# Kernel tuning notes

Measured on AMD Instinct MI355X. Metric: run time of the kernel, lower is better.

Reference implementation:

```python
import jax, jax.numpy as jnp
import numpy as np

B, S, D, H = 2, 2048, 2048, 16
DH = D // H  # 128


def setup_inputs() -> dict:
    key = jax.random.key(0)
    ks = jax.random.split(key, 7)
    x = jax.random.normal(ks[0], (B, S, D), dtype=jnp.float32)
    # causal mask [b, s, s], True = attend
    mask = jnp.broadcast_to(jnp.tril(jnp.ones((S, S), dtype=bool)), (B, S, S))
    scale = 1.0 / np.sqrt(D)
    Wq = jax.random.normal(ks[1], (D, H, DH), dtype=jnp.float32) * scale
    Wk = jax.random.normal(ks[2], (D, 1, DH), dtype=jnp.float32) * scale
    Wv = jax.random.normal(ks[3], (D, 1, DH), dtype=jnp.float32) * scale
    Wo = jax.random.normal(ks[4], (H, DH, D), dtype=jnp.float32) * scale
    bo = jnp.zeros((D,), dtype=jnp.float32)
    return {"x": x, "mask": mask, "Wq": Wq, "Wk": Wk, "Wv": Wv, "Wo": Wo, "bo": bo}


def reference(x, mask, Wq, Wk, Wv, Wo, bo):
    # projections: q [b,s,h,dh]; k,v [b,s,1,dh] (single shared KV head)
    q = jnp.einsum("bsd,dhe->bshe", x, Wq)
    k = jnp.einsum("bsd,dhe->bshe", x, Wk)[:, :, 0, :]  # [b,s,dh]
    v = jnp.einsum("bsd,dhe->bshe", x, Wv)[:, :, 0, :]  # [b,s,dh]
    # scores [b,h,s,s] with 1/sqrt(d_head) scaling
    scores = jnp.einsum("bqhe,bke->bhqk", q, k) / jnp.sqrt(
        jnp.asarray(q.shape[-1], dtype=q.dtype)
    )
    big_neg = jnp.finfo(scores.dtype).min
    scores = jnp.where(mask[:, None, :, :], scores, big_neg)
    probs = jax.nn.softmax(scores, axis=-1)
    attn = jnp.einsum("bhqk,bke->bhqe", probs, v)  # [b,h,s,dh]
    # output projection contracting (head, d_head) -> d_state, with bias
    out = jnp.einsum("bhqe,hed->bqd", attn, Wo) + bo
    return out
```

## Files before the change

kernel.cpp:

```cpp
#include <hip/hip_runtime.h>
#include <cmath>
#include <cstdint>

typedef __bf16 bf16;
typedef __bf16 bf16x8 __attribute__((ext_vector_type(8)));
typedef __bf16 bf16x4 __attribute__((ext_vector_type(4)));
typedef float f32x4 __attribute__((ext_vector_type(4)));

#define SDIM 2048
#define DDIM 2048
#define NQKV 2304
#define DH   128

__device__ __forceinline__ void glds16(const bf16* g, bf16* l) {
    __builtin_amdgcn_global_load_lds(
        (const __attribute__((address_space(1))) void*)g,
        (__attribute__((address_space(3))) void*)l, 16, 0, 0);
}

#define MEMFENCE() asm volatile("" ::: "memory")
#define SBAR() do { MEMFENCE(); __builtin_amdgcn_s_barrier(); MEMFENCE(); } while (0)

__global__ __launch_bounds__(256) void prep_kernel(const float* __restrict__ x,
                                                   const float* __restrict__ Wq,
                                                   const float* __restrict__ Wk,
                                                   const float* __restrict__ Wv,
                                                   const float* __restrict__ Wo,
                                                   bf16* __restrict__ xb,
                                                   bf16* __restrict__ Wqkv_t,
                                                   bf16* __restrict__ Wo_t) {
    __shared__ float tile[32][33];
    int bx = blockIdx.x;
    if (bx < 8192) {
        int i = bx * 256 + threadIdx.x;
        float4 v = reinterpret_cast<const float4*>(x)[i];
        bf16x4 o;
        o[0] = (bf16)v.x; o[1] = (bf16)v.y; o[2] = (bf16)v.z; o[3] = (bf16)v.w;
        reinterpret_cast<bf16x4*>(xb)[i] = o;
        return;
    }
    bx -= 8192;
    const float* src; bf16* dst; int srcN; int t;
    if (bx < 4096)      { src = Wq; dst = Wqkv_t;                      srcN = 2048; t = bx; }
    else if (bx < 4352) { src = Wk; dst = Wqkv_t + (size_t)2048*2048;  srcN = 128;  t = bx - 4096; }
    else if (bx < 4608) { src = Wv; dst = Wqkv_t + (size_t)2176*2048;  srcN = 128;  t = bx - 4352; }
    else                { src = Wo; dst = Wo_t;                        srcN = 2048; t = bx - 4608; }
    const int srcK = 2048;
    int ntx = srcN >> 5;
    int n0 = (t % ntx) * 32, k0 = (t / ntx) * 32;
    int tx = threadIdx.x & 31;
    int ty = threadIdx.x >> 5;
    for (int i = 0; i < 4; i++)
        tile[ty + i*8][tx] = src[(size_t)(k0 + ty + i*8) * srcN + n0 + tx];
    __syncthreads();
    for (int i = 0; i < 4; i++)
        dst[(size_t)(n0 + ty + i*8) * srcK + k0 + tx] = (bf16)tile[tx][ty + i*8];
}

template<int WRITE_F32, int BNW, int WRITE_VT>
__global__ __launch_bounds__(512, 2) void gemm8_kernel(const bf16* __restrict__ A,
                                                       const bf16* __restrict__ Bt,
                                                       void* __restrict__ Cout,
                                                       const float* __restrict__ bias,
                                                       bf16* __restrict__ Vt,
                                                       int N) {
    constexpr int K  = 2048;
    constexpr int NT = 32;
    constexpr int BN = 64 * BNW;
    constexpr int BHALF = BN * 32;
    __shared__ bf16 smem[32768 + 4 * BHALF];

    const int tid  = threadIdx.x;
    const int wave = tid >> 6, lane = tid & 63;
    const int quad = lane >> 4, l15 = lane & 15;
    const int wm = wave >> 2, wn = wave & 3;
    const int tm = blockIdx.x * 256, tn = blockIdx.y * BN;

    const int r0  = wave * 32 + (lane >> 2);
    const int r0b = (BNW == 4) ? r0 : (wave * 16 + (lane >> 2));
    const int cs  = (lane & 3) ^ ((lane >> 3) & 3);
    const bf16* Ag = A  + (size_t)(tm + r0)  * K + cs * 8;
    const bf16* Bg = Bt + (size_t)(tn + r0b) * K + cs * 8;
    bf16* Asl = smem + wave * 1024;
    bf16* Bsl = smem + 32768 + wave * ((BNW == 4) ? 1024 : 512);

    auto STAGE_A = [&](int t, int kh) {
        if (t < NT) {
            const bf16* s = Ag + t * 64 + kh * 32;
            bf16* d = Asl + (t & 1) * 16384 + kh * 8192;
            glds16(s, d);
            glds16(s + 16 * K, d + 512);
        }
    };
    auto STAGE_B = [&](int t, int kh) {
        if (t < NT) {
            const bf16* s = Bg + t * 64 + kh * 32;
            bf16* d = Bsl + (t & 1) * (2 * BHALF) + kh * BHALF;
            glds16(s, d);
            if constexpr (BNW == 4) glds16(s + 16 * K, d + 512);
        }
    };

    const int rsw  = (l15 >> 1) & 3;
    const int aoff = (wm * 128      + l15) * 32 + ((quad ^ rsw) * 8);
    const int boff = (wn * 16 * BNW + l15) * 32 + ((quad ^ rsw) * 8);

    f32x4 acc[8][BNW];
#pragma unroll
    for (int m = 0; m < 8; m++)
#pragma unroll
        for (int n = 0; n < BNW; n++) acc[m][n] = (f32x4)0.0f;

    STAGE_A(0, 0); STAGE_B(0, 0);
    STAGE_A(0, 1); STAGE_B(0, 1);
    STAGE_A(1, 0); STAGE_B(1, 0);
    if constexpr (BNW == 4) asm volatile("s_waitcnt vmcnt(4)" ::: "memory");
    else                    asm volatile("s_waitcnt vmcnt(3)" ::: "memory");
    SBAR();

    bf16x8 av[4], bv[BNW];
    for (int t = 0; t < NT; ++t) {
        const int buf = t & 1;
        const bf16* Sa = smem + buf * 16384;
        const bf16* Sb = smem + 32768 + buf * (2 * BHALF);

#pragma unroll
        for (int m = 0; m < 4; m++) av[m] = *reinterpret_cast<const bf16x8*>(Sa + aoff + m * 512);
#pragma unroll
        for (int n = 0; n < BNW; n++) bv[n] = *reinterpret_cast<const bf16x8*>(Sb + boff + n * 512);
        STAGE_A(t + 1, 1);
        SBAR();
        __builtin_amdgcn_s_setprio(1);
#pragma unroll
        for (int m = 0; m < 4; m++)
#pragma unroll
            for (int n = 0; n < BNW; n++)
                acc[m][n] = __builtin_amdgcn_mfma_f32_16x16x32_bf16(av[m], bv[n], acc[m][n], 0, 0, 0);
        __builtin_amdgcn_s_setprio(0);
        SBAR();

#pragma unroll
        for (int m = 0; m < 4; m++) av[m] = *reinterpret_cast<const bf16x8*>(Sa + aoff + 2048 + m * 512);
        STAGE_B(t + 1, 1);
        SBAR();
        __builtin_amdgcn_s_setprio(1);
#pragma unroll
        for (int m = 0; m < 4; m++)
#pragma unroll
            for (int n = 0; n < BNW; n++)
                acc[4 + m][n] = __builtin_amdgcn_mfma_f32_16x16x32_bf16(av[m], bv[n], acc[4 + m][n], 0, 0, 0);
        __builtin_amdgcn_s_setprio(0);
        if (t + 1 < NT) {
            if constexpr (BNW == 4) asm volatile("s_waitcnt vmcnt(8)" ::: "memory");
            else                    asm volatile("s_waitcnt vmcnt(6)" ::: "memory");
        } else {
            asm volatile("s_waitcnt vmcnt(0)" ::: "memory");
        }
        SBAR();

#pragma unroll
        for (int m = 0; m < 4; m++) av[m] = *reinterpret_cast<const bf16x8*>(Sa + 8192 + aoff + m * 512);
#pragma unroll
        for (int n = 0; n < BNW; n++) bv[n] = *reinterpret_cast<const bf16x8*>(Sb + BHALF + boff + n * 512);
        STAGE_A(t + 2, 0);
        SBAR();
        __builtin_amdgcn_s_setprio(1);
#pragma unroll
        for (int m = 0; m < 4; m++)
#pragma unroll
            for (int n = 0; n < BNW; n++)
                acc[m][n] = __builtin_amdgcn_mfma_f32_16x16x32_bf16(av[m], bv[n], acc[m][n], 0, 0, 0);
        __builtin_amdgcn_s_setprio(0);
        SBAR();

#pragma unroll
        for (int m = 0; m < 4; m++) av[m] = *reinterpret_cast<const bf16x8*>(Sa + 8192 + aoff + 2048 + m * 512);
        STAGE_B(t + 2, 0);
        SBAR();
        __builtin_amdgcn_s_setprio(1);
#pragma unroll
        for (int m = 0; m < 4; m++)
#pragma unroll
            for (int n = 0; n < BNW; n++)
                acc[4 + m][n] = __builtin_amdgcn_mfma_f32_16x16x32_bf16(av[m], bv[n], acc[4 + m][n], 0, 0, 0);
        __builtin_amdgcn_s_setprio(0);
        if (t + 2 < NT) {
            if constexpr (BNW == 4) asm volatile("s_waitcnt vmcnt(4)" ::: "memory");
            else                    asm volatile("s_waitcnt vmcnt(3)" ::: "memory");
        } else {
            asm volatile("s_waitcnt vmcnt(0)" ::: "memory");
        }
        SBAR();
    }

#pragma unroll
    for (int m = 0; m < 8; m++)
#pragma unroll
        for (int n = 0; n < BNW; n++) {
#pragma unroll
            for (int r = 0; r < 4; r++) {
                int row = tm + wm * 128 + m * 16 + quad * 4 + r;
                int col = tn + wn * 16 * BNW + n * 16 + l15;
                float v = acc[m][n][r];
                if (WRITE_F32)
                    reinterpret_cast<float*>(Cout)[(size_t)row * N + col] = v + bias[col];
                else
                    reinterpret_cast<bf16*>(Cout)[(size_t)row * N + col] = (bf16)v;
            }
            if constexpr (WRITE_VT) {
                if (tn == 2048 && wn >= 2) {
                    int col  = tn + wn * 16 * BNW + n * 16 + l15;
                    int d    = col - 2176;
                    int row0 = tm + wm * 128 + m * 16 + quad * 4;
                    int bb   = row0 >> 11;
                    int s0v  = row0 & 2047;
                    int pp0  = (s0v & ~63) | (s0v & 32) | ((s0v & 12) << 1) | ((s0v & 16) >> 2);
                    bf16x4 vv;
                    vv[0] = (bf16)acc[m][n][0]; vv[1] = (bf16)acc[m][n][1];
                    vv[2] = (bf16)acc[m][n][2]; vv[3] = (bf16)acc[m][n][3];
                    *reinterpret_cast<bf16x4*>(Vt + ((size_t)bb * DH + d) * SDIM + pp0) = vv;
                }
            }
        }
}

__global__ __launch_bounds__(512, 4) void flash_kernel(const bf16* __restrict__ QKV,
                                                       const bf16* __restrict__ Vt,
                                                       bf16* __restrict__ attn) {
    __shared__ __align__(16) bf16 KVS[32768];
    const int tid  = threadIdx.x;
    const int wave = tid >> 6, lane = tid & 63;
    const int quad = lane >> 4, l15 = lane & 15;
    const int bx = blockIdx.x;
    const int u  = (bx < 256) ? bx : bx - 256;
    const int qs = (bx < 256) ? (255 - (u >> 1)) : (u >> 1);
    const int b  = u & 1;
    const int q  = qs * 8 + wave;
    const size_t rowbase = (size_t)b * SDIM;
    const bf16* Vtb = Vt + (size_t)b * DH * SDIM;
    const float scale = 0.088388347648318447f;

    const int s0 = wave, s1 = wave + 8;
    const int krow0 = s0*4 + quad, krow1 = s1*4 + quad;
    const bf16* kp0 = QKV + (rowbase + krow0) * NQKV + 2048 + ((l15 ^ (krow0 & 15)) * 8);
    const bf16* kp1 = QKV + (rowbase + krow1) * NQKV + 2048 + ((l15 ^ (krow1 & 15)) * 8);
    const int vrow0 = s0*8 + (lane >> 3), vrow1 = s1*8 + (lane >> 3);
    const bf16* vp0 = Vtb + (size_t)vrow0 * SDIM + (((lane & 7) ^ (vrow0 & 7)) * 8);
    const bf16* vp1 = Vtb + (size_t)vrow1 * SDIM + (((lane & 7) ^ (vrow1 & 7)) * 8);

    bf16x8 qf[4];
    {
        const bf16* qp = QKV + (rowbase + q) * NQKV + l15 * DH + quad * 8;
#pragma unroll
        for (int kk = 0; kk < 4; kk++) qf[kk] = *reinterpret_cast<const bf16x8*>(qp + kk * 32);
    }

    f32x4 acc[8];
#pragma unroll
    for (int d = 0; d < 8; d++) acc[d] = (f32x4)0.0f;
    float l_s = 0.0f;

    const int ntiles = (qs >> 3) + 1;

    glds16(kp0, KVS + s0 * 512);         glds16(kp1, KVS + s1 * 512);
    glds16(vp0, KVS + 16384 + s0 * 512); glds16(vp1, KVS + 16384 + s1 * 512);
    kp0 += 64 * NQKV; kp1 += 64 * NQKV; vp0 += 64; vp1 += 64;

    for (int t = 0; t < ntiles; t++) {
        asm volatile("s_waitcnt vmcnt(2)" ::: "memory");
        SBAR();
        if (t + 1 < ntiles) {
            bf16* kb = KVS + ((t + 1) & 1) * 8192;
            glds16(kp0, kb + s0 * 512); glds16(kp1, kb + s1 * 512);
            kp0 += 64 * NQKV; kp1 += 64 * NQKV;
        }
        const bf16* Ks  = KVS + (t & 1) * 8192;
        const bf16* Vts = KVS + 16384 + (t & 1) * 8192;
        const int key0 = t * 64;

        f32x4 sc[4];
#pragma unroll
        for (int c = 0; c < 4; c++) sc[c] = (f32x4)0.0f;
        __builtin_amdgcn_s_setprio(1);
#pragma unroll
        for (int c = 0; c < 4; c++)
#pragma unroll
            for (int kk = 0; kk < 4; kk++) {
                bf16x8 kf = *reinterpret_cast<const bf16x8*>(
                    Ks + (c*16 + l15) * 128 + (((kk*4 + quad) ^ l15) * 8));
                sc[c] = __builtin_amdgcn_mfma_f32_16x16x32_bf16(kf, qf[kk], sc[c], 0, 0, 0);
            }
        __builtin_amdgcn_s_setprio(0);

        bf16x8 pa[2];
        {
            const bool tail = (key0 + 63 > q);
            float ps = 0.0f;
#pragma unroll
            for (int c = 0; c < 4; c++)
#pragma unroll
                for (int r = 0; r < 4; r++) {
                    int key = key0 + c*16 + quad*4 + r;
                    float pv = (tail && key > q) ? 0.0f : __expf(sc[c][r] * scale);
                    ps += pv;
                    pa[c >> 1][(c & 1)*4 + r] = (bf16)pv;
                }
            l_s += ps;
        }

        if (t + 1 < ntiles) asm volatile("s_waitcnt vmcnt(2)" ::: "memory");
        else                asm volatile("s_waitcnt vmcnt(0)" ::: "memory");

        __builtin_amdgcn_s_setprio(1);
#pragma unroll
        for (int kk2 = 0; kk2 < 2; kk2++)
#pragma unroll
            for (int dd = 0; dd < 8; dd++) {
                bf16x8 vf = *reinterpret_cast<const bf16x8*>(
                    Vts + (dd*16 + l15) * 64 + (((kk2*4 + quad) ^ (l15 & 7)) * 8));
                acc[dd] = __builtin_amdgcn_mfma_f32_16x16x32_bf16(pa[kk2], vf, acc[dd], 0, 0, 0);
            }
        __builtin_amdgcn_s_setprio(0);

        if (t + 1 < ntiles) {
            bf16* vb = KVS + 16384 + ((t + 1) & 1) * 8192;
            glds16(vp0, vb + s0 * 512); glds16(vp1, vb + s1 * 512);
            vp0 += 64; vp1 += 64;
        }
    }

    __syncthreads();

    float linv;
    {
        float v = l_s;
        v += __shfl_xor(v, 16);
        v += __shfl_xor(v, 32);
        linv = 1.0f / v;
    }

    bf16* Ow = KVS + wave * 2048;
#pragma unroll
    for (int r = 0; r < 4; r++) {
        float inv = __shfl(linv, quad*4 + r);
#pragma unroll
        for (int dd = 0; dd < 8; dd++)
            Ow[(quad*4 + r)*128 + dd*16 + l15] = (bf16)(acc[dd][r] * inv);
    }
    const int orow = lane >> 2;
    const int ocol = (lane & 3) * 8;
    bf16* ob = attn + (rowbase + q) * (size_t)DDIM;
#pragma unroll
    for (int it = 0; it < 4; it++)
        *reinterpret_cast<uint4*>(ob + orow * DH + ocol + it*32) =
            *reinterpret_cast<const uint4*>(Ow + orow * 128 + ocol + it*32);
}

extern "C" void kernel_launch(void* const* d_in, const int* in_sizes, int n_in,
                              void* d_out, int out_size, void* d_ws, size_t ws_size,
                              hipStream_t stream) {
    const float* x  = (const float*)d_in[0];
    const float* Wq = (const float*)d_in[2];
    const float* Wk = (const float*)d_in[3];
    const float* Wv = (const float*)d_in[4];
    const float* Wo = (const float*)d_in[5];
    const float* bo = (const float*)d_in[6];
    float* out = (float*)d_out;

    char* ws = (char*)d_ws;
    bf16* xb     = (bf16*)(ws);
    bf16* Wqkv_t = (bf16*)(ws + 16777216);
    bf16* Wo_t   = (bf16*)(ws + 26214400);
    bf16* QKV    = (bf16*)(ws + 34603008);
    bf16* attn   = (bf16*)(ws + 53477376);
    bf16* Vtb    = (bf16*)(ws + 70254592);
    (void)ws_size; (void)in_sizes; (void)n_in; (void)out_size;

    prep_kernel<<<16896, 256, 0, stream>>>(x, Wq, Wk, Wv, Wo, xb, Wqkv_t, Wo_t);
    gemm8_kernel<0, 4, 1><<<dim3(16, 9), 512, 0, stream>>>(xb, Wqkv_t, (void*)QKV, nullptr, Vtb, 2304);
    flash_kernel<<<512, 512, 0, stream>>>(QKV, Vtb, attn);
    gemm8_kernel<1, 2, 0><<<dim3(16, 16), 512, 0, stream>>>(attn, Wo_t, (void*)out, bo, nullptr, 2048);
}
```

Measured before the change: 281.8 us.

## Restructure GEMM main loop into a triple-buffered K=32 pipeline with one barrier

The GEMM main loop changes from a double-buffered 64-wide K step, split into four sub-phases with many barriers, to a triple-buffered 32-wide K step. Each iteration issues the async global-to-LDS load two steps ahead, runs all 8xBNW MFMAs, then waits and crosses a single barrier. This aims to cut barrier and synchronisation overhead and keep more loads in flight. The cost is more loop iterations, a different LDS footprint, and register pressure from holding 8 A fragments at once.

```diff
diff --git a/kernel.cpp b/kernel.cpp
--- a/kernel.cpp
+++ b/kernel.cpp
@@ -58,52 +58,45 @@
 }
 
 template<int WRITE_F32, int BNW, int WRITE_VT>
-__global__ __launch_bounds__(512, 2) void gemm8_kernel(const bf16* __restrict__ A,
+__global__ __launch_bounds__(512, 2) void gemm9_kernel(const bf16* __restrict__ A,
                                                        const bf16* __restrict__ Bt,
                                                        void* __restrict__ Cout,
                                                        const float* __restrict__ bias,
                                                        bf16* __restrict__ Vt,
                                                        int N) {
-    constexpr int K  = 2048;
-    constexpr int NT = 32;
-    constexpr int BN = 64 * BNW;
-    constexpr int BHALF = BN * 32;
-    __shared__ bf16 smem[32768 + 4 * BHALF];
+    constexpr int K    = 2048;
+    constexpr int NT   = 64;
+    constexpr int ABUF = 8192;
+    constexpr int BBUF = BNW * 2048;
+    constexpr int GPT  = 2 + (BNW >> 1);
+    __shared__ bf16 smem[3 * ABUF + 3 * BBUF];
 
     const int tid  = threadIdx.x;
     const int wave = tid >> 6, lane = tid & 63;
     const int quad = lane >> 4, l15 = lane & 15;
     const int wm = wave >> 2, wn = wave & 3;
-    const int tm = blockIdx.x * 256, tn = blockIdx.y * BN;
-
-    const int r0  = wave * 32 + (lane >> 2);
-    const int r0b = (BNW == 4) ? r0 : (wave * 16 + (lane >> 2));
-    const int cs  = (lane & 3) ^ ((lane >> 3) & 3);
-    const bf16* Ag = A  + (size_t)(tm + r0)  * K + cs * 8;
-    const bf16* Bg = Bt + (size_t)(tn + r0b) * K + cs * 8;
-    bf16* Asl = smem + wave * 1024;
-    bf16* Bsl = smem + 32768 + wave * ((BNW == 4) ? 1024 : 512);
-
-    auto STAGE_A = [&](int t, int kh) {
-        if (t < NT) {
-            const bf16* s = Ag + t * 64 + kh * 32;
-            bf16* d = Asl + (t & 1) * 16384 + kh * 8192;
-            glds16(s, d);
-            glds16(s + 16 * K, d + 512);
-        }
+    const int tm = blockIdx.x * 256, tn = blockIdx.y * (64 * BNW);
+
+    const int rr = wave * 16 + (lane >> 2);
+    const int cs = (lane & 3) ^ ((lane >> 3) & 3);
+    const bf16* Ag = A  + (size_t)(tm + rr) * K + cs * 8;
+    const bf16* Bg = Bt + (size_t)(tn + rr) * K + cs * 8;
+    bf16* Asl = smem + wave * 512;
+    bf16* Bsl = smem + 3 * ABUF + wave * 512;
+
+    auto STAGE = [&](int t, int s3) {
+        const bf16* sa = Ag + t * 32;
+        bf16* da = Asl + s3 * ABUF;
+        glds16(sa, da);
+        glds16(sa + 128 * K, da + 4096);
+        const bf16* sb = Bg + t * 32;
+        bf16* db = Bsl + s3 * BBUF;
+        glds16(sb, db);
+        if constexpr (BNW == 4) glds16(sb + 128 * K, db + 4096);
     };
-    auto STAGE_B = [&](int t, int kh) {
-        if (t < NT) {
-            const bf16* s = Bg + t * 64 + kh * 32;
-            bf16* d = Bsl + (t & 1) * (2 * BHALF) + kh * BHALF;
-            glds16(s, d);
-            if constexpr (BNW == 4) glds16(s + 16 * K, d + 512);
-        }
-    };
 
     const int rsw  = (l15 >> 1) & 3;
-    const int aoff = (wm * 128      + l15) * 32 + ((quad ^ rsw) * 8);
-    const int boff = (wn * 16 * BNW + l15) * 32 + ((quad ^ rsw) * 8);
+    const int coff = (quad ^ rsw) * 8;
 
     f32x4 acc[8][BNW];
 #pragma unroll
@@ -111,79 +104,34 @@
 #pragma unroll
         for (int n = 0; n < BNW; n++) acc[m][n] = (f32x4)0.0f;
 
-    STAGE_A(0, 0); STAGE_B(0, 0);
-    STAGE_A(0, 1); STAGE_B(0, 1);
-    STAGE_A(1, 0); STAGE_B(1, 0);
+    STAGE(0, 0);
+    STAGE(1, 1);
     if constexpr (BNW == 4) asm volatile("s_waitcnt vmcnt(4)" ::: "memory");
     else                    asm volatile("s_waitcnt vmcnt(3)" ::: "memory");
     SBAR();
 
-    bf16x8 av[4], bv[BNW];
+    int b3 = 0, s3 = 2;
     for (int t = 0; t < NT; ++t) {
-        const int buf = t & 1;
-        const bf16* Sa = smem + buf * 16384;
-        const bf16* Sb = smem + 32768 + buf * (2 * BHALF);
-
-#pragma unroll
-        for (int m = 0; m < 4; m++) av[m] = *reinterpret_cast<const bf16x8*>(Sa + aoff + m * 512);
-#pragma unroll
-        for (int n = 0; n < BNW; n++) bv[n] = *reinterpret_cast<const bf16x8*>(Sb + boff + n * 512);
-        STAGE_A(t + 1, 1);
-        SBAR();
+        if (t + 2 < NT) STAGE(t + 2, s3);
+
+        const bf16* Ab = smem + b3 * ABUF;
+        const bf16* Bb = smem + 3 * ABUF + b3 * BBUF;
+        bf16x8 av[8], bv[BNW];
+#pragma unroll
+        for (int m = 0; m < 8; m++)
+            av[m] = *reinterpret_cast<const bf16x8*>(Ab + (wm*128 + m*16 + l15) * 32 + coff);
+#pragma unroll
+        for (int n = 0; n < BNW; n++)
+            bv[n] = *reinterpret_cast<const bf16x8*>(Bb + (wn*16*BNW + n*16 + l15) * 32 + coff);
+
         __builtin_amdgcn_s_setprio(1);
 #pragma unroll
-        for (int m = 0; m < 4; m++)
+        for (int m = 0; m < 8; m++)
 #pragma unroll
             for (int n = 0; n < BNW; n++)
                 acc[m][n] = __builtin_amdgcn_mfma_f32_16x16x32_bf16(av[m], bv[n], acc[m][n], 0, 0, 0);
         __builtin_amdgcn_s_setprio(0);
-        SBAR();
-
-#pragma unroll
-        for (int m = 0; m < 4; m++) av[m] = *reinterpret_cast<const bf16x8*>(Sa + aoff + 2048 + m * 512);
-        STAGE_B(t + 1, 1);
-        SBAR();
-        __builtin_amdgcn_s_setprio(1);
-#pragma unroll
-        for (int m = 0; m < 4; m++)
-#pragma unroll
-            for (int n = 0; n < BNW; n++)
-                acc[4 + m][n] = __builtin_amdgcn_mfma_f32_16x16x32_bf16(av[m], bv[n], acc[4 + m][n], 0, 0, 0);
-        __builtin_amdgcn_s_setprio(0);
-        if (t + 1 < NT) {
-            if constexpr (BNW == 4) asm volatile("s_waitcnt vmcnt(8)" ::: "memory");
-            else                    asm volatile("s_waitcnt vmcnt(6)" ::: "memory");
-        } else {
-            asm volatile("s_waitcnt vmcnt(0)" ::: "memory");
-        }
-        SBAR();
-
-#pragma unroll
-        for (int m = 0; m < 4; m++) av[m] = *reinterpret_cast<const bf16x8*>(Sa + 8192 + aoff + m * 512);
-#pragma unroll
-        for (int n = 0; n < BNW; n++) bv[n] = *reinterpret_cast<const bf16x8*>(Sb + BHALF + boff + n * 512);
-        STAGE_A(t + 2, 0);
-        SBAR();
-        __builtin_amdgcn_s_setprio(1);
-#pragma unroll
-        for (int m = 0; m < 4; m++)
-#pragma unroll
-            for (int n = 0; n < BNW; n++)
-                acc[m][n] = __builtin_amdgcn_mfma_f32_16x16x32_bf16(av[m], bv[n], acc[m][n], 0, 0, 0);
-        __builtin_amdgcn_s_setprio(0);
-        SBAR();
-
-#pragma unroll
-        for (int m = 0; m < 4; m++) av[m] = *reinterpret_cast<const bf16x8*>(Sa + 8192 + aoff + 2048 + m * 512);
-        STAGE_B(t + 2, 0);
-        SBAR();
-        __builtin_amdgcn_s_setprio(1);
-#pragma unroll
-        for (int m = 0; m < 4; m++)
-#pragma unroll
-            for (int n = 0; n < BNW; n++)
-                acc[4 + m][n] = __builtin_amdgcn_mfma_f32_16x16x32_bf16(av[m], bv[n], acc[4 + m][n], 0, 0, 0);
-        __builtin_amdgcn_s_setprio(0);
+
         if (t + 2 < NT) {
             if constexpr (BNW == 4) asm volatile("s_waitcnt vmcnt(4)" ::: "memory");
             else                    asm volatile("s_waitcnt vmcnt(3)" ::: "memory");
@@ -191,6 +139,8 @@
             asm volatile("s_waitcnt vmcnt(0)" ::: "memory");
         }
         SBAR();
+        b3 = (b3 == 2) ? 0 : b3 + 1;
+        s3 = (s3 == 2) ? 0 : s3 + 1;
     }
 
 #pragma unroll
@@ -377,7 +327,7 @@
     (void)ws_size; (void)in_sizes; (void)n_in; (void)out_size;
 
     prep_kernel<<<16896, 256, 0, stream>>>(x, Wq, Wk, Wv, Wo, xb, Wqkv_t, Wo_t);
-    gemm8_kernel<0, 4, 1><<<dim3(16, 9), 512, 0, stream>>>(xb, Wqkv_t, (void*)QKV, nullptr, Vtb, 2304);
+    gemm9_kernel<0, 4, 1><<<dim3(16, 9), 512, 0, stream>>>(xb, Wqkv_t, (void*)QKV, nullptr, Vtb, 2304);
     flash_kernel<<<512, 512, 0, stream>>>(QKV, Vtb, attn);
-    gemm8_kernel<1, 2, 0><<<dim3(16, 16), 512, 0, stream>>>(attn, Wo_t, (void*)out, bo, nullptr, 2048);
-}
+    gemm9_kernel<1, 2, 0><<<dim3(16, 16), 512, 0, stream>>>(attn, Wo_t, (void*)out, bo, nullptr, 2048);
+}
```

Measured after the change: 280.9 us. Within noise of the previous version (-0.3%).
